# Kernel optimization log

Measured on AMD Instinct MI355X. Metric: run time of the kernel, lower is better.

The kernel has to match this reference:

```python
import jax, jax.numpy as jnp
import numpy as np

WS = 8   # window_size
SS = 4   # shift_size
NH = 4   # num_heads


def _window_partition(x, w):
    B, H, W, C = x.shape
    x = x.reshape(B, H // w, w, W // w, w, C).transpose(0, 1, 3, 2, 4, 5)
    return x.reshape(-1, w, w, C)


def _window_reverse(win, w, H, W):
    B = win.shape[0] // ((H // w) * (W // w))
    x = win.reshape(B, H // w, W // w, w, w, -1).transpose(0, 1, 3, 2, 4, 5)
    return x.reshape(B, H, W, -1)


def _rel_pos_index(w):
    coords = np.stack(np.meshgrid(np.arange(w), np.arange(w), indexing='ij'))  # (2,w,w)
    cf = coords.reshape(2, -1)
    rel = cf[:, :, None] - cf[:, None, :]          # (2,N,N)
    rel = rel.transpose(1, 2, 0)                   # (N,N,2)
    rel[:, :, 0] += w - 1
    rel[:, :, 1] += w - 1
    rel[:, :, 0] *= 2 * w - 1
    return rel.sum(-1)                             # (N,N) int


def _attn_mask(Hp, Wp, w, ss):
    if ss == 0:
        return None
    img = np.zeros((1, Hp, Wp, 1), np.float32)
    slices = (slice(0, -w), slice(-w, -ss), slice(-ss, None))
    cnt = 0
    for h in slices:
        for ww in slices:
            img[:, h, ww, :] = cnt
            cnt += 1
    mw = img.reshape(1, Hp // w, w, Wp // w, w, 1).transpose(0, 1, 3, 2, 4, 5).reshape(-1, w * w)
    m = mw[:, None, :] - mw[:, :, None]
    return np.where(m != 0, -100.0, 0.0).astype(np.float32)  # (nW,N,N)


def _ln(x, g, b, eps=1e-5):
    mu = x.mean(-1, keepdims=True)
    var = ((x - mu) ** 2).mean(-1, keepdims=True)
    return (x - mu) * jax.lax.rsqrt(var + eps) * g + b


def setup_inputs() -> dict:
    key = jax.random.key(0)
    ks = jax.random.split(key, 8)
    B, H, W, C = 4, 256, 256, 128
    hid = 4 * C
    s = 0.02
    return {
        'x': jax.random.normal(ks[0], (B, H * W, C), jnp.float32),
        'norm1_g': jnp.ones((C,), jnp.float32),
        'norm1_b': jnp.zeros((C,), jnp.float32),
        'qkv_w': jax.random.normal(ks[1], (3 * C, C), jnp.float32) * s,
        'qkv_b': jnp.zeros((3 * C,), jnp.float32),
        'rpb_table': jax.random.normal(ks[2], ((2 * WS - 1) ** 2, NH), jnp.float32) * s,
        'proj_w': jax.random.normal(ks[3], (C, C), jnp.float32) * s,
        'proj_b': jnp.zeros((C,), jnp.float32),
        'norm2_g': jnp.ones((C,), jnp.float32),
        'norm2_b': jnp.zeros((C,), jnp.float32),
        'fc1_w': jax.random.normal(ks[4], (hid, C), jnp.float32) * s,
        'fc1_b': jnp.zeros((hid,), jnp.float32),
        'fc2_w': jax.random.normal(ks[5], (C, hid), jnp.float32) * s,
        'fc2_b': jnp.zeros((C,), jnp.float32),
        'H': H,
        'W': W,
    }


def reference(x, norm1_g, norm1_b, qkv_w, qkv_b, rpb_table, proj_w, proj_b,
              norm2_g, norm2_b, fc1_w, fc1_b, fc2_w, fc2_b, H, W):
    B, L, C = x.shape
    hd = C // NH
    scale = hd ** -0.5
    N = WS * WS

    shortcut = x
    h = _ln(x, norm1_g, norm1_b).reshape(B, H, W, C)

    pad_r = (WS - W % WS) % WS
    pad_b = (WS - H % WS) % WS
    if pad_r > 0 or pad_b > 0:
        h = jnp.pad(h, ((0, 0), (0, pad_b), (0, pad_r), (0, 0)))
    Hp, Wp = H + pad_b, W + pad_r

    if SS > 0:
        h = jnp.roll(h, (-SS, -SS), axis=(1, 2))

    win = _window_partition(h, WS).reshape(-1, N, C)   # (B_,N,C)
    B_ = win.shape[0]

    qkv = (win @ qkv_w.T + qkv_b).reshape(B_, N, 3, NH, hd).transpose(2, 0, 3, 1, 4)
    q, k, v = qkv[0] * scale, qkv[1], qkv[2]           # (B_,NH,N,hd)

    attn = jnp.einsum('whnd,whmd->whnm', q, k)         # (B_,NH,N,N)
    rpi = _rel_pos_index(WS).reshape(-1)
    bias = rpb_table[rpi].reshape(N, N, NH).transpose(2, 0, 1)
    attn = attn + bias[None]

    mask = _attn_mask(Hp, Wp, WS, SS)
    if mask is not None:
        nW = mask.shape[0]
        attn = attn.reshape(B_ // nW, nW, NH, N, N) + jnp.asarray(mask)[None, :, None]
        attn = attn.reshape(B_, NH, N, N)

    attn = jax.nn.softmax(attn, axis=-1)
    out = jnp.einsum('whnm,whmd->whnd', attn, v).transpose(0, 2, 1, 3).reshape(B_, N, C)
    out = out @ proj_w.T + proj_b

    out = _window_reverse(out.reshape(-1, WS, WS, C), WS, Hp, Wp)
    if SS > 0:
        out = jnp.roll(out, (SS, SS), axis=(1, 2))
    if pad_r > 0 or pad_b > 0:
        out = out[:, :H, :W, :]
    x = shortcut + out.reshape(B, H * W, C)

    y = _ln(x, norm2_g, norm2_b)
    y = jax.nn.gelu(y @ fc1_w.T + fc1_b, approximate=False) @ fc2_w.T + fc2_b
    return x + y
```

## Files before the change

kernel.cpp:

```cpp
#include <hip/hip_runtime.h>
#include <hip/hip_bf16.h>

typedef unsigned short u16;
typedef unsigned int u32;
typedef __attribute__((ext_vector_type(8))) short bf16x8;
typedef __attribute__((ext_vector_type(4))) float f32x4;

__device__ __forceinline__ u32 fbits(float f) { union { float f; u32 u; } a; a.f = f; return a.u; }
__device__ __forceinline__ u16 f2bf(float f) {
    u32 u = fbits(f);
    return (u16)((u + 0x7FFFu + ((u >> 16) & 1u)) >> 16);
}
__device__ __forceinline__ u16 bfr(float f) { return (u16)((fbits(f) + 0x8000u) >> 16); }
__device__ __forceinline__ u32 pk2(float lo, float hi) {
    return __builtin_amdgcn_perm(fbits(hi) + 0x8000u, fbits(lo) + 0x8000u, 0x07060302u);
}
__device__ __forceinline__ float bf2f(u16 b) {
    union { u32 u; float f; } a; a.u = ((u32)b) << 16; return a.f;
}
__device__ __forceinline__ float gelu_poly(float t) {
    float u = fminf(3.0f, fmaxf(-3.0f, t));
    float u2 = u * u;
    float w = fmaf(u2, 0.00319581f, -0.0550159f);
    w = fmaf(u2, w, 0.401174f);
    float sg = fmaf(u, w, 0.5f);
    return t * sg;
}

#define MFMA(a, b, c) __builtin_amdgcn_mfma_f32_16x16x32_bf16(a, b, c, 0, 0, 0)

__device__ __forceinline__ void gload16(const u16* g, u16* l) {
    __builtin_amdgcn_global_load_lds(
        (const __attribute__((address_space(1))) void*)g,
        (__attribute__((address_space(3))) void*)l, 16, 0, 0);
}

__global__ void swin_prep_kernel(const float* __restrict__ qkv_w, const float* __restrict__ proj_w,
                                 const float* __restrict__ fc1_w, const float* __restrict__ fc2_w,
                                 const float* __restrict__ rpb, u16* __restrict__ wout,
                                 float* __restrict__ bias_lane)
{
    int idx = blockIdx.x * 256 + threadIdx.x;
    if (idx < 49152) wout[idx] = f2bf(qkv_w[idx]);
    else if (idx < 81920) {
        int j = idx - 49152;
        int tile = j >> 9, lane = (j >> 3) & 63, e = j & 7;
        int nt = tile >> 2, ks = tile & 3;
        wout[idx] = f2bf(proj_w[(nt * 16 + (lane & 15)) * 128 + ks * 32 + (lane >> 4) * 8 + e]);
    } else if (idx < 212992) {
        int j = idx - 81920;
        int chunk = j >> 13, rest = j & 8191;
        int tile = rest >> 9, lane = (rest >> 3) & 63, e = rest & 7;
        int lg = lane >> 4;
        float v;
        if (tile < 8) {
            int mh = tile >> 2, ks = tile & 3;
            v = fc1_w[(chunk * 32 + mh * 16 + (lane & 15)) * 128 + ks * 32 + lg * 8 + e];
        } else {
            int nt = tile - 8;
            int hid = (e < 4) ? (lg * 4 + e) : (16 + lg * 4 + (e - 4));
            v = fc2_w[(nt * 16 + (lane & 15)) * 512 + chunk * 32 + hid];
        }
        wout[idx] = f2bf(v);
    } else {
        int t = idx - 212992;
        int r = t & 3, lane = (t >> 2) & 63, nt = (t >> 8) & 3, mt = (t >> 10) & 3;
        int h = (t >> 12) & 3, v = (t >> 14) & 3;
        int i = mt * 16 + (lane & 15);
        int j = nt * 16 + ((lane >> 4) << 2) + r;
        int ri = i >> 3, ci = i & 7, rj = j >> 3, cj = j & 7;
        int rpi = (ri - rj + 7) * 15 + (ci - cj + 7);
        float bv = rpb[rpi * 4 + h];
        int vh = v >> 1, vw = v & 1;
        int regi = (vh ? (ri < 4 ? 1 : 2) : 0) * 3 + (vw ? (ci < 4 ? 1 : 2) : 0);
        int regj = (vh ? (rj < 4 ? 1 : 2) : 0) * 3 + (vw ? (cj < 4 ? 1 : 2) : 0);
        if (regi != regj) bv -= 100.0f;
        bias_lane[t] = bv * 1.4426950408889634f;
    }
}

__global__ __launch_bounds__(512, 4) void swin_attn_kernel(
    const float* __restrict__ x, const float* __restrict__ g1, const float* __restrict__ b1,
    const float* __restrict__ qkvb, const u16* __restrict__ qkvw,
    const float* __restrict__ bias_lane, u16* __restrict__ attn_out)
{
    __shared__ __align__(16) u16 ldsX[8448];
    __shared__ __align__(16) u16 ldsQK[16896];
    __shared__ float sb[640];

    int tid = threadIdx.x;
    int wid = blockIdx.x;
    int bb_ = wid >> 10, wh = (wid >> 5) & 31, ww = wid & 31;

    for (int i = tid; i < 640; i += 512) {
        float v;
        if (i < 128) v = g1[i];
        else if (i < 256) v = b1[i - 128];
        else v = qkvb[i - 256];
        sb[i] = v;
    }

    int trow = tid >> 3, seg = tid & 7;
    int rn = trow >> 3, cn = trow & 7;
    int srow = (wh * 8 + rn + 4) & 255;
    int scol = (ww * 8 + cn + 4) & 255;
    long grow = (long)bb_ * 65536 + srow * 256 + scol;
    const float4* xrow = (const float4*)(x + grow * 128 + seg * 16);
    float4 xv[4];
    #pragma unroll
    for (int i = 0; i < 4; ++i) xv[i] = xrow[i];
    __syncthreads();

    float s1 = 0.0f, s2 = 0.0f;
    #pragma unroll
    for (int i = 0; i < 4; ++i) {
        float4 v = xv[i];
        s1 += v.x + v.y + v.z + v.w;
        s2 += v.x * v.x + v.y * v.y + v.z * v.z + v.w * v.w;
    }
    #pragma unroll
    for (int off = 1; off < 8; off <<= 1) { s1 += __shfl_xor(s1, off); s2 += __shfl_xor(s2, off); }
    float mu = s1 * 0.0078125f;
    float rstd = rsqrtf(s2 * 0.0078125f - mu * mu + 1e-5f);
    {
        u32 pk[8];
        #pragma unroll
        for (int i = 0; i < 4; ++i) {
            float vv[4] = {xv[i].x, xv[i].y, xv[i].z, xv[i].w};
            float y0, y1, y2, y3;
            {
                int c = seg * 16 + i * 4;
                y0 = (vv[0] - mu) * rstd * sb[c + 0] + sb[128 + c + 0];
                y1 = (vv[1] - mu) * rstd * sb[c + 1] + sb[128 + c + 1];
                y2 = (vv[2] - mu) * rstd * sb[c + 2] + sb[128 + c + 2];
                y3 = (vv[3] - mu) * rstd * sb[c + 3] + sb[128 + c + 3];
            }
            pk[i * 2]     = pk2(y0, y1);
            pk[i * 2 + 1] = pk2(y2, y3);
        }
        *(uint4*)&ldsX[trow * 132 + seg * 16] = *(uint4*)&pk[0];
        *(uint4*)&ldsX[trow * 132 + seg * 16 + 8] = *(uint4*)&pk[4];
    }
    __syncthreads();

    int wave = tid >> 6, lane = tid & 63, l15 = lane & 15, lg = lane >> 4;
    int mrow = lg * 4;
    bf16x8 afr[4][4];
    #pragma unroll
    for (int mt = 0; mt < 4; ++mt)
        #pragma unroll
        for (int ks = 0; ks < 4; ++ks)
            afr[mt][ks] = *(const bf16x8*)&ldsX[(mt * 16 + l15) * 132 + ks * 32 + lg * 8];
    __syncthreads();
    #pragma unroll 1
    for (int nn = 0; nn < 3; ++nn) {
        int nt = wave * 3 + nn;
        int n = nt * 16 + l15;
        const u16* wp = qkvw + n * 128 + lg * 8;
        bf16x8 bfr_[4];
        #pragma unroll
        for (int ks = 0; ks < 4; ++ks) bfr_[ks] = *(const bf16x8*)(wp + ks * 32);
        f32x4 acc[4];
        #pragma unroll
        for (int mt = 0; mt < 4; ++mt) acc[mt] = (f32x4){0.0f, 0.0f, 0.0f, 0.0f};
        #pragma unroll
        for (int ks = 0; ks < 4; ++ks)
            #pragma unroll
            for (int mt = 0; mt < 4; ++mt)
                acc[mt] = MFMA(afr[mt][ks], bfr_[ks], acc[mt]);
        float bias = sb[256 + n];
        if (n < 128) {
            #pragma unroll
            for (int mt = 0; mt < 4; ++mt)
                #pragma unroll
                for (int r = 0; r < 4; ++r)
                    ldsQK[(mt * 16 + mrow + r) * 132 + n] = bfr(acc[mt][r] + bias);
        } else if (n < 256) {
            #pragma unroll
            for (int mt = 0; mt < 4; ++mt)
                #pragma unroll
                for (int r = 0; r < 4; ++r)
                    ldsQK[8448 + (mt * 16 + mrow + r) * 132 + (n - 128)] = bfr(acc[mt][r] + bias);
        } else {
            int row = n - 256;
            int sw = (row & 7) << 4;
            #pragma unroll
            for (int mt = 0; mt < 4; ++mt) {
                uint2 pv;
                pv.x = pk2(acc[mt][0] + bias, acc[mt][1] + bias);
                pv.y = pk2(acc[mt][2] + bias, acc[mt][3] + bias);
                int cb = ((mt >> 1) * 64 + mrow * 4 + (mt & 1) * 8) ^ sw;
                *(uint2*)((char*)ldsX + row * 128 + cb) = pv;
            }
        }
    }
    __syncthreads();

    int h = wave >> 1, half = wave & 1;
    int v4 = ((wh == 31) ? 2 : 0) | ((ww == 31) ? 1 : 0);
    const float4* blp = (const float4*)bias_lane;
    bf16x8 bk[4];
    #pragma unroll
    for (int nt = 0; nt < 4; ++nt)
        bk[nt] = *(const bf16x8*)&ldsQK[8448 + (nt * 16 + l15) * 132 + h * 32 + lg * 8];
    bf16x8 aq[2];
    #pragma unroll
    for (int m2 = 0; m2 < 2; ++m2)
        aq[m2] = *(const bf16x8*)&ldsQK[((half * 2 + m2) * 16 + l15) * 132 + h * 32 + lg * 8];
    f32x4 sS[2][4];
    #pragma unroll
    for (int m2 = 0; m2 < 2; ++m2) {
        int mt = half * 2 + m2;
        #pragma unroll
        for (int nt = 0; nt < 4; ++nt) {
            f32x4 z = (f32x4){0.0f, 0.0f, 0.0f, 0.0f};
            z = MFMA(bk[nt], aq[m2], z);
            float4 bl = blp[((v4 * 4 + h) * 16 + mt * 4 + nt) * 64 + lane];
            sS[m2][nt][0] = z[0] * 0.2550349f + bl.x;
            sS[m2][nt][1] = z[1] * 0.2550349f + bl.y;
            sS[m2][nt][2] = z[2] * 0.2550349f + bl.z;
            sS[m2][nt][3] = z[3] * 0.2550349f + bl.w;
        }
    }
    float rinv[2];
    #pragma unroll
    for (int m2 = 0; m2 < 2; ++m2) {
        float sum = 0.0f;
        #pragma unroll
        for (int nt = 0; nt < 4; ++nt)
            #pragma unroll
            for (int r = 0; r < 4; ++r) {
                float p = exp2f(sS[m2][nt][r]);
                sS[m2][nt][r] = p;
                sum += p;
            }
        sum += __shfl_xor(sum, 16);
        sum += __shfl_xor(sum, 32);
        rinv[m2] = __builtin_amdgcn_rcpf(sum);
    }
    f32x4 o[2][2];
    #pragma unroll
    for (int m2 = 0; m2 < 2; ++m2)
        #pragma unroll
        for (int np = 0; np < 2; ++np) o[m2][np] = (f32x4){0.0f, 0.0f, 0.0f, 0.0f};
    #pragma unroll
    for (int kt = 0; kt < 2; ++kt) {
        bf16x8 pa[2];
        #pragma unroll
        for (int m2 = 0; m2 < 2; ++m2) {
            union { u32 w[4]; bf16x8 v; } u_;
            u_.w[0] = pk2(sS[m2][2 * kt][0], sS[m2][2 * kt][1]);
            u_.w[1] = pk2(sS[m2][2 * kt][2], sS[m2][2 * kt][3]);
            u_.w[2] = pk2(sS[m2][2 * kt + 1][0], sS[m2][2 * kt + 1][1]);
            u_.w[3] = pk2(sS[m2][2 * kt + 1][2], sS[m2][2 * kt + 1][3]);
            pa[m2] = u_.v;
        }
        #pragma unroll
        for (int np = 0; np < 2; ++np) {
            int vr = h * 32 + np * 16 + l15;
            int cb = (kt * 64 + lg * 16) ^ ((vr & 7) << 4);
            bf16x8 bv = *(const bf16x8*)((const char*)ldsX + vr * 128 + cb);
            #pragma unroll
            for (int m2 = 0; m2 < 2; ++m2)
                o[m2][np] = MFMA(pa[m2], bv, o[m2][np]);
        }
    }
    __syncthreads();
    #pragma unroll
    for (int m2 = 0; m2 < 2; ++m2) {
        int mt = half * 2 + m2;
        #pragma unroll
        for (int np = 0; np < 2; ++np)
            #pragma unroll
            for (int r = 0; r < 4; ++r) {
                float rq = __shfl(rinv[m2], lg * 4 + r);
                ldsX[(mt * 16 + mrow + r) * 132 + h * 32 + np * 16 + l15] = bfr(o[m2][np][r] * rq);
            }
    }
    __syncthreads();
    u16* op = attn_out + grow * 128 + seg * 16;
    *(uint4*)op = *(const uint4*)&ldsX[trow * 132 + seg * 16];
    *(uint4*)(op + 8) = *(const uint4*)&ldsX[trow * 132 + seg * 16 + 8];
}

__global__ __launch_bounds__(256, 3) void swin_mlp_kernel(
    const u16* __restrict__ attn, const float* __restrict__ x,
    const u16* __restrict__ projws, const u16* __restrict__ wms,
    const float* __restrict__ projb, const float* __restrict__ g2, const float* __restrict__ b2,
    const float* __restrict__ f1b, const float* __restrict__ f2b, float* __restrict__ out)
{
    __shared__ __align__(16) u16 wbuf[2][8192];
    __shared__ __align__(16) u16 sbuf[4][576];

    int tid = threadIdx.x;
    int wave = tid >> 6, lane = tid & 63, l15 = lane & 15, lg = lane >> 4;
    long wbase = (long)blockIdx.x * 128 + wave * 32;

    {
        const u16* src = wms + wave * 2048 + lane * 8;
        u16* dst = &wbuf[0][wave * 2048];
        #pragma unroll
        for (int i = 0; i < 4; ++i)
            gload16(src + i * 512, dst + i * 512);
    }

    const u16* arow = attn + (wbase + l15) * 128 + lg * 8;
    bf16x8 aat[2][4];
    #pragma unroll
    for (int ks = 0; ks < 4; ++ks) {
        aat[0][ks] = *(const bf16x8*)(arow + ks * 32);
        aat[1][ks] = *(const bf16x8*)(arow + 2048 + ks * 32);
    }

    f32x4 pacc[2][8];
    #pragma unroll
    for (int nt = 0; nt < 8; ++nt) {
        const u16* wp = projws + nt * 2048 + lane * 8;
        pacc[0][nt] = (f32x4){0.0f, 0.0f, 0.0f, 0.0f};
        pacc[1][nt] = (f32x4){0.0f, 0.0f, 0.0f, 0.0f};
        #pragma unroll
        for (int ks = 0; ks < 4; ++ks) {
            bf16x8 bw = *(const bf16x8*)(wp + ks * 512);
            pacc[0][nt] = MFMA(aat[0][ks], bw, pacc[0][nt]);
            pacc[1][nt] = MFMA(aat[1][ks], bw, pacc[1][nt]);
        }
    }

    #pragma unroll
    for (int nt = 0; nt < 8; ++nt) {
        float pb = projb[nt * 16 + l15];
        #pragma unroll
        for (int mt = 0; mt < 2; ++mt)
            #pragma unroll
            for (int r = 0; r < 4; ++r)
                pacc[mt][nt][r] += x[(wbase + mt * 16 + lg * 4 + r) * 128 + nt * 16 + l15] + pb;
    }
    float mu[2][4], rstd[2][4];
    #pragma unroll
    for (int mt = 0; mt < 2; ++mt)
        #pragma unroll
        for (int r = 0; r < 4; ++r) {
            float a = 0.0f, bq = 0.0f;
            #pragma unroll
            for (int nt = 0; nt < 8; ++nt) { a += pacc[mt][nt][r]; bq += pacc[mt][nt][r] * pacc[mt][nt][r]; }
            #pragma unroll
            for (int off = 1; off < 16; off <<= 1) { a += __shfl_xor(a, off); bq += __shfl_xor(bq, off); }
            mu[mt][r] = a * 0.0078125f;
            rstd[mt][r] = rsqrtf(bq * 0.0078125f - mu[mt][r] * mu[mt][r] + 1e-5f);
        }
    u16* hb = (u16*)sbuf[wave];
    bf16x8 ay[2][4];
    #pragma unroll
    for (int p = 0; p < 4; ++p) {
        #pragma unroll
        for (int mt = 0; mt < 2; ++mt) {
            #pragma unroll
            for (int n2 = 0; n2 < 2; ++n2) {
                int c = p * 32 + n2 * 16 + l15;
                float gg = g2[c], bb = b2[c];
                int nt = p * 2 + n2;
                #pragma unroll
                for (int r = 0; r < 4; ++r)
                    hb[(lg * 4 + r) * 36 + n2 * 16 + l15] =
                        bfr((pacc[mt][nt][r] - mu[mt][r]) * rstd[mt][r] * gg + bb);
            }
            __builtin_amdgcn_sched_barrier(0);
            ay[mt][p] = *(const bf16x8*)&hb[l15 * 36 + lg * 8];
            __builtin_amdgcn_sched_barrier(0);
        }
    }
    #pragma unroll
    for (int nt = 0; nt < 8; ++nt) {
        float fb = f2b[nt * 16 + l15];
        #pragma unroll
        for (int mt = 0; mt < 2; ++mt)
            #pragma unroll
            for (int r = 0; r < 4; ++r)
                pacc[mt][nt][r] += fb;
    }
    __syncthreads();

    #pragma unroll 1
    for (int cc = 0; cc < 16; ++cc) {
        int cur = cc & 1;
        if (cc < 15) {
            const u16* src = wms + (cc + 1) * 8192 + wave * 2048 + lane * 8;
            u16* dst = &wbuf[cur ^ 1][wave * 2048];
            #pragma unroll
            for (int i = 0; i < 4; ++i)
                gload16(src + i * 512, dst + i * 512);
        }
        f32x4 h[2][2];
        h[0][0] = h[0][1] = h[1][0] = h[1][1] = (f32x4){0.0f, 0.0f, 0.0f, 0.0f};
        #pragma unroll
        for (int mh = 0; mh < 2; ++mh)
            #pragma unroll
            for (int ks = 0; ks < 4; ++ks) {
                bf16x8 w1 = *(const bf16x8*)&wbuf[cur][(mh * 4 + ks) * 512 + lane * 8];
                h[0][mh] = MFMA(w1, ay[0][ks], h[0][mh]);
                h[1][mh] = MFMA(w1, ay[1][ks], h[1][mh]);
            }
        float4 fb0 = *(const float4*)(f1b + cc * 32 + lg * 4);
        float4 fb1 = *(const float4*)(f1b + cc * 32 + 16 + lg * 4);
        float b0[4] = {fb0.x, fb0.y, fb0.z, fb0.w};
        float b1[4] = {fb1.x, fb1.y, fb1.z, fb1.w};
        bf16x8 ah[2];
        #pragma unroll
        for (int mt = 0; mt < 2; ++mt) {
            float g0[4], g1[4];
            #pragma unroll
            for (int r = 0; r < 4; ++r) {
                g0[r] = gelu_poly(h[mt][0][r] + b0[r]);
                g1[r] = gelu_poly(h[mt][1][r] + b1[r]);
            }
            union { u32 w[4]; bf16x8 v; } u_;
            u_.w[0] = pk2(g0[0], g0[1]);
            u_.w[1] = pk2(g0[2], g0[3]);
            u_.w[2] = pk2(g1[0], g1[1]);
            u_.w[3] = pk2(g1[2], g1[3]);
            ah[mt] = u_.v;
        }
        #pragma unroll
        for (int nt = 0; nt < 8; ++nt) {
            bf16x8 bw = *(const bf16x8*)&wbuf[cur][(8 + nt) * 512 + lane * 8];
            pacc[0][nt] = MFMA(ah[0], bw, pacc[0][nt]);
            pacc[1][nt] = MFMA(ah[1], bw, pacc[1][nt]);
        }
        __syncthreads();
    }
    #pragma unroll
    for (int nt = 0; nt < 8; ++nt)
        #pragma unroll
        for (int mt = 0; mt < 2; ++mt)
            #pragma unroll
            for (int r = 0; r < 4; ++r)
                out[(wbase + mt * 16 + lg * 4 + r) * 128 + nt * 16 + l15] = pacc[mt][nt][r];
}

extern "C" void kernel_launch(void* const* d_in, const int* in_sizes, int n_in,
                              void* d_out, int out_size, void* d_ws, size_t ws_size,
                              hipStream_t stream)
{
    const float* x     = (const float*)d_in[0];
    const float* n1g   = (const float*)d_in[1];
    const float* n1b   = (const float*)d_in[2];
    const float* qkvw  = (const float*)d_in[3];
    const float* qkvb  = (const float*)d_in[4];
    const float* rpb   = (const float*)d_in[5];
    const float* projw = (const float*)d_in[6];
    const float* projb = (const float*)d_in[7];
    const float* n2g   = (const float*)d_in[8];
    const float* n2b   = (const float*)d_in[9];
    const float* f1w   = (const float*)d_in[10];
    const float* f1b   = (const float*)d_in[11];
    const float* f2w   = (const float*)d_in[12];
    const float* f2b   = (const float*)d_in[13];

    char* ws = (char*)d_ws;
    u16* attn_buf = (u16*)ws;
    u16* wb = (u16*)(ws + 67108864);
    float* bias_lane = (float*)(ws + 67108864 + 425984);
    u16* qkvwb  = wb;
    u16* projws = wb + 49152;
    u16* wms    = wb + 81920;

    swin_prep_kernel<<<1088, 256, 0, stream>>>(qkvw, projw, f1w, f2w, rpb, wb, bias_lane);
    swin_attn_kernel<<<4096, 512, 0, stream>>>(x, n1g, n1b, qkvb, qkvwb, bias_lane, attn_buf);
    swin_mlp_kernel<<<2048, 256, 0, stream>>>(attn_buf, x, projws, wms,
                                              projb, n2g, n2b, f1b, f2b, (float*)d_out);
}
```

Measured before the change: 230.6 us.

## Triple-buffer MLP weight chunks with partial vmcnt waits and LDS bias

The fused MLP kernel now keeps three LDS weight buffers, prefetching two chunks ahead instead of one. Per-iteration full syncthreads is replaced by s_waitcnt vmcnt(4) plus a raw barrier, so only the oldest chunk's loads must land before proceeding. The fc1 bias is staged once into LDS, and the layernorm scratch reuses the third weight buffer. LDS use grows from about 37KB to about 50KB per block, which may lower occupancy under launch_bounds(256,3), and the hand-counted vmcnt values depend on gload16 issuing exactly four loads per chunk.

```diff
diff --git a/kernel.cpp b/kernel.cpp
--- a/kernel.cpp
+++ b/kernel.cpp
@@ -289,8 +289,8 @@
     const float* __restrict__ projb, const float* __restrict__ g2, const float* __restrict__ b2,
     const float* __restrict__ f1b, const float* __restrict__ f2b, float* __restrict__ out)
 {
-    __shared__ __align__(16) u16 wbuf[2][8192];
-    __shared__ __align__(16) u16 sbuf[4][576];
+    __shared__ __align__(16) u16 wbuf[3][8192];
+    __shared__ __align__(16) float f1s[512];
 
     int tid = threadIdx.x;
     int wave = tid >> 6, lane = tid & 63, l15 = lane & 15, lg = lane >> 4;
@@ -298,11 +298,15 @@
 
     {
         const u16* src = wms + wave * 2048 + lane * 8;
-        u16* dst = &wbuf[0][wave * 2048];
         #pragma unroll
         for (int i = 0; i < 4; ++i)
-            gload16(src + i * 512, dst + i * 512);
-    }
+            gload16(src + i * 512, &wbuf[0][wave * 2048] + i * 512);
+        #pragma unroll
+        for (int i = 0; i < 4; ++i)
+            gload16(src + 8192 + i * 512, &wbuf[1][wave * 2048] + i * 512);
+    }
+    f1s[tid] = f1b[tid];
+    f1s[tid + 256] = f1b[tid + 256];
 
     const u16* arow = attn + (wbase + l15) * 128 + lg * 8;
     bf16x8 aat[2][4];
@@ -348,7 +352,7 @@
             mu[mt][r] = a * 0.0078125f;
             rstd[mt][r] = rsqrtf(bq * 0.0078125f - mu[mt][r] * mu[mt][r] + 1e-5f);
         }
-    u16* hb = (u16*)sbuf[wave];
+    u16* hb = &wbuf[2][wave * 2048];
     bf16x8 ay[2][4];
     #pragma unroll
     for (int p = 0; p < 4; ++p) {
@@ -378,30 +382,33 @@
             for (int r = 0; r < 4; ++r)
                 pacc[mt][nt][r] += fb;
     }
-    __syncthreads();
-
+    asm volatile("s_waitcnt vmcnt(4)" ::: "memory");
+    __builtin_amdgcn_s_barrier();
+    __builtin_amdgcn_sched_barrier(0);
+
+    int cur = 0, pre = 2;
     #pragma unroll 1
     for (int cc = 0; cc < 16; ++cc) {
-        int cur = cc & 1;
-        if (cc < 15) {
-            const u16* src = wms + (cc + 1) * 8192 + wave * 2048 + lane * 8;
-            u16* dst = &wbuf[cur ^ 1][wave * 2048];
+        if (cc < 14) {
+            const u16* src = wms + (cc + 2) * 8192 + wave * 2048 + lane * 8;
+            u16* dst = &wbuf[pre][wave * 2048];
             #pragma unroll
             for (int i = 0; i < 4; ++i)
                 gload16(src + i * 512, dst + i * 512);
         }
+        const u16* wc = &wbuf[cur][0];
         f32x4 h[2][2];
         h[0][0] = h[0][1] = h[1][0] = h[1][1] = (f32x4){0.0f, 0.0f, 0.0f, 0.0f};
         #pragma unroll
         for (int mh = 0; mh < 2; ++mh)
             #pragma unroll
             for (int ks = 0; ks < 4; ++ks) {
-                bf16x8 w1 = *(const bf16x8*)&wbuf[cur][(mh * 4 + ks) * 512 + lane * 8];
+                bf16x8 w1 = *(const bf16x8*)(wc + (mh * 4 + ks) * 512 + lane * 8);
                 h[0][mh] = MFMA(w1, ay[0][ks], h[0][mh]);
                 h[1][mh] = MFMA(w1, ay[1][ks], h[1][mh]);
             }
-        float4 fb0 = *(const float4*)(f1b + cc * 32 + lg * 4);
-        float4 fb1 = *(const float4*)(f1b + cc * 32 + 16 + lg * 4);
+        float4 fb0 = *(const float4*)&f1s[cc * 32 + lg * 4];
+        float4 fb1 = *(const float4*)&f1s[cc * 32 + 16 + lg * 4];
         float b0[4] = {fb0.x, fb0.y, fb0.z, fb0.w};
         float b1[4] = {fb1.x, fb1.y, fb1.z, fb1.w};
         bf16x8 ah[2];
@@ -422,11 +429,18 @@
         }
         #pragma unroll
         for (int nt = 0; nt < 8; ++nt) {
-            bf16x8 bw = *(const bf16x8*)&wbuf[cur][(8 + nt) * 512 + lane * 8];
+            bf16x8 bw = *(const bf16x8*)(wc + (8 + nt) * 512 + lane * 8);
             pacc[0][nt] = MFMA(ah[0], bw, pacc[0][nt]);
             pacc[1][nt] = MFMA(ah[1], bw, pacc[1][nt]);
         }
-        __syncthreads();
+        if (cc < 15) {
+            if (cc < 14) asm volatile("s_waitcnt vmcnt(4)" ::: "memory");
+            else         asm volatile("s_waitcnt vmcnt(0)" ::: "memory");
+            __builtin_amdgcn_s_barrier();
+            __builtin_amdgcn_sched_barrier(0);
+        }
+        cur = (cur == 2) ? 0 : cur + 1;
+        pre = (pre == 2) ? 0 : pre + 1;
     }
     #pragma unroll
     for (int nt = 0; nt < 8; ++nt)
```

Result: faster. 224.0 us (-2.9%).
